# Performance work log

Hardware: AMD Instinct MI355X
Metric: run time of the kernel (lower is better)

## Reference

```python
import jax, jax.numpy as jnp
import numpy as np

K = 3
PAD = 1
DG = 4
GN_GROUPS = 32
EPS = 1e-5


def deform_conv2d(x, offset, weight):
    # x: [B,C,H,W], offset: [B,DG*2*K*K,H,W] (mmcv layout: per group, per kernel tap, (dy,dx))
    B, C, H, W = x.shape
    KK = K * K
    cg = C // DG
    dt = x.dtype
    off = offset.reshape(B, DG, KK, 2, H, W)
    dy, dx = off[:, :, :, 0], off[:, :, :, 1]  # [B,DG,KK,H,W]
    ky, kx = jnp.meshgrid(jnp.arange(K), jnp.arange(K), indexing='ij')
    ky = ky.reshape(KK).astype(dt)
    kx = kx.reshape(KK).astype(dt)
    hh = jnp.arange(H, dtype=dt)
    ww = jnp.arange(W, dtype=dt)
    # sampling coords: p0 + p_k + offset (stride 1, dilation 1)
    y = hh[None, None, None, :, None] - PAD + ky[None, None, :, None, None] + dy
    xs = ww[None, None, None, None, :] - PAD + kx[None, None, :, None, None] + dx
    y0 = jnp.floor(y)
    x0 = jnp.floor(xs)
    wy1 = y - y0
    wx1 = xs - x0
    xg = x.reshape(B, DG, cg, H * W)

    def corner(yi, xi):
        # zero padding outside the feature map
        valid = (yi >= 0) & (yi < H) & (xi >= 0) & (xi < W)
        yc = jnp.clip(yi, 0, H - 1).astype(jnp.int32)
        xc = jnp.clip(xi, 0, W - 1).astype(jnp.int32)
        idx = (yc * W + xc).reshape(B, DG, KK * H * W)
        v = jax.vmap(jax.vmap(lambda xf, ix: xf[:, ix]))(xg, idx)  # [B,DG,cg,KK*H*W]
        v = v.reshape(B, DG, cg, KK, H, W)
        return v * valid.astype(dt)[:, :, None]

    col = (corner(y0, x0) * ((1 - wy1) * (1 - wx1))[:, :, None]
           + corner(y0, x0 + 1) * ((1 - wy1) * wx1)[:, :, None]
           + corner(y0 + 1, x0) * (wy1 * (1 - wx1))[:, :, None]
           + corner(y0 + 1, x0 + 1) * (wy1 * wx1)[:, :, None])  # [B,DG,cg,KK,H,W]
    col = col.reshape(B, C, KK, H, W)
    O = weight.shape[0]
    return jnp.einsum('ock,bckhw->bohw', weight.reshape(O, C, KK), col)


def group_norm(x, gamma, beta):
    B, C, H, W = x.shape
    xg = x.reshape(B, GN_GROUPS, -1)
    m = xg.mean(-1, keepdims=True)
    v = xg.var(-1, keepdims=True)
    xn = ((xg - m) * jax.lax.rsqrt(v + EPS)).reshape(B, C, H, W)
    return xn * gamma[None, :, None, None] + beta[None, :, None, None]


def setup_inputs() -> dict:
    key = jax.random.key(0)
    k1, k2, k3, k4 = jax.random.split(key, 4)
    B, C, H, W = 4, 256, 64, 64
    x = jax.random.normal(k1, (B, C, H, W), dtype=jnp.float32)
    shape = jax.random.normal(k2, (B, 4, H, W), dtype=jnp.float32)
    w_offset = jax.random.normal(k3, (DG * 2 * K * K, 4), dtype=jnp.float32) * 0.01
    w_deform = jax.random.normal(k4, (C, C, K, K), dtype=jnp.float32) * 0.01
    gamma = jnp.ones((C,), jnp.float32)
    beta = jnp.zeros((C,), jnp.float32)
    return {"x": x, "shape": shape, "w_offset": w_offset, "w_deform": w_deform, "gamma": gamma, "beta": beta}


def reference(x, shape, w_offset, w_deform, gamma, beta):
    # conv_offset: 1x1 conv on detached `shape`
    offset = jnp.einsum('oi,bihw->bohw', w_offset, jax.lax.stop_gradient(shape))
    out = deform_conv2d(x, offset, w_deform)
    return jax.nn.relu(group_norm(out, gamma, beta))
```

## Files before the change

### kernel.cpp

```cpp
#include <hip/hip_runtime.h>
#include <stdint.h>

#define BB   4
#define CCH  256
#define HH   64
#define WWD  64
#define HWSZ 4096
#define DGRP 4
#define CG   64
#define KKN  9
#define KT   2304
#define NND  16384
#define GNG  32
#define EPSV 1e-5f

#define WS_COLT  0
#define WS_WB    75497472
#define WS_G     76677120
#define WS_PART  93454336

typedef __attribute__((ext_vector_type(8))) short short8;
typedef __attribute__((ext_vector_type(4))) float f32x4;

__device__ inline unsigned short f2bf(float f) {
    union { float f; unsigned u; } v; v.f = f;
    unsigned u = v.u;
    return (unsigned short)((u + 0x7FFFu + ((u >> 16) & 1u)) >> 16);
}

__device__ inline void gl_lds16(const void* g, void* l) {
    __builtin_amdgcn_global_load_lds(
        (const __attribute__((address_space(1))) void*)g,
        (__attribute__((address_space(3))) void*)l,
        16, 0, 0);
}

__global__ __launch_bounds__(256) void wconv_kernel(const float* __restrict__ wd,
                                                    unsigned short* __restrict__ Wb) {
    int idx = blockIdx.x * 256 + threadIdx.x;
    int o = idx / KT;
    int r = idx % KT;
    int kk = r >> 8;
    int c  = r & 255;
    Wb[idx] = f2bf(wd[o * KT + c * KKN + kk]);
}

__global__ __launch_bounds__(256) void col_kernel(const float* __restrict__ x,
                                                  const float* __restrict__ shp,
                                                  const float* __restrict__ woff,
                                                  unsigned short* __restrict__ colT) {
    __shared__ __align__(16) float xt[4 * 12 * 64 * 4];

    int bid   = blockIdx.x;
    int band  = bid & 7;
    int cq    = (bid >> 3) & 3;
    int dg    = (bid >> 5) & 3;
    int b     = bid >> 7;
    int h0    = band * 8;
    int tid   = threadIdx.x;
    int lane  = tid & 63;
    int wv    = tid >> 6;

    const float* xg = x + (size_t)(b * CCH + dg * CG + cq * 16) * HWSZ;
    #pragma unroll 1
    for (int ii = 0; ii < 6; ++ii) {
        float v[8]; int la[8];
        #pragma unroll
        for (int u = 0; u < 8; ++u) {
            int idx = (ii * 8 + u) * 256 + tid;
            int j   = idx / 768;
            int rem = idx - j * 768;
            int r   = rem >> 6;
            int w   = rem & 63;
            int gr  = min(max(h0 - 2 + r, 0), HH - 1);
            v[u]  = xg[(size_t)j * HWSZ + gr * 64 + w];
            la[u] = ((j >> 2) * 12 + r) * 256 + w * 4 + (j & 3);
        }
        #pragma unroll
        for (int u = 0; u < 8; ++u) xt[la[u]] = v[u];
    }
    __syncthreads();

    const char* xtb = (const char*)xt;

    #pragma unroll 1
    for (int hr = 0; hr < 2; ++hr) {
        int h  = h0 + wv * 2 + hr;
        int hw = h * 64 + lane;
        float s0 = shp[(b * 4 + 0) * HWSZ + hw];
        float s1 = shp[(b * 4 + 1) * HWSZ + hw];
        float s2 = shp[(b * 4 + 2) * HWSZ + hw];
        float s3 = shp[(b * 4 + 3) * HWSZ + hw];

        unsigned short* rowp = colT + (size_t)(b * HWSZ + hw) * KT + dg * CG + cq * 16;

        #pragma unroll
        for (int kk = 0; kk < KKN; ++kk) {
            const float* wo = woff + (dg * 18 + kk * 2) * 4;
            float dy = wo[0] * s0 + wo[1] * s1 + wo[2] * s2 + wo[3] * s3;
            float dx = wo[4] * s0 + wo[5] * s1 + wo[6] * s2 + wo[7] * s3;

            int ky = kk / 3, kx = kk % 3;
            float y  = (float)(h - 1 + ky) + dy;
            float xs = (float)(lane - 1 + kx) + dx;
            float y0f = floorf(y), x0f = floorf(xs);
            float wy1 = y - y0f,  wx1 = xs - x0f;
            float wy0 = 1.f - wy1, wx0 = 1.f - wx1;
            int iy0 = (int)y0f, ix0 = (int)x0f;
            int iy1 = iy0 + 1,  ix1 = ix0 + 1;
            bool vy0 = (iy0 >= 0) && (iy0 < HH);
            bool vy1 = (iy1 >= 0) && (iy1 < HH);
            bool vx0 = (ix0 >= 0) && (ix0 < WWD);
            bool vx1 = (ix1 >= 0) && (ix1 < WWD);
            float w00 = (vy0 && vx0) ? wy0 * wx0 : 0.f;
            float w01 = (vy0 && vx1) ? wy0 * wx1 : 0.f;
            float w10 = (vy1 && vx0) ? wy1 * wx0 : 0.f;
            float w11 = (vy1 && vx1) ? wy1 * wx1 : 0.f;
            int cy0 = min(max(iy0, 0), HH - 1);
            int cy1 = min(max(iy1, 0), HH - 1);
            int cx0 = min(max(ix0, 0), WWD - 1);
            int cx1 = min(max(ix1, 0), WWD - 1);
            int ty0 = min(max(cy0 - (h0 - 2), 0), 11);
            int ty1 = min(max(cy1 - (h0 - 2), 0), 11);
            int a00 = (ty0 * 64 + cx0) * 16;
            int a01 = (ty0 * 64 + cx1) * 16;
            int a10 = (ty1 * 64 + cx0) * 16;
            int a11 = (ty1 * 64 + cx1) * 16;

            unsigned short tmp[16];
            #pragma unroll
            for (int c4g = 0; c4g < 4; ++c4g) {
                int base = c4g * 12288;
                const float4 v00 = *(const float4*)(xtb + base + a00);
                const float4 v01 = *(const float4*)(xtb + base + a01);
                const float4 v10 = *(const float4*)(xtb + base + a10);
                const float4 v11 = *(const float4*)(xtb + base + a11);
                float rx = w00 * v00.x + w01 * v01.x + w10 * v10.x + w11 * v11.x;
                float ry = w00 * v00.y + w01 * v01.y + w10 * v10.y + w11 * v11.y;
                float rz = w00 * v00.z + w01 * v01.z + w10 * v10.z + w11 * v11.z;
                float rw = w00 * v00.w + w01 * v01.w + w10 * v10.w + w11 * v11.w;
                tmp[c4g * 4 + 0] = f2bf(rx);
                tmp[c4g * 4 + 1] = f2bf(ry);
                tmp[c4g * 4 + 2] = f2bf(rz);
                tmp[c4g * 4 + 3] = f2bf(rw);
            }
            uint4* dst = (uint4*)(rowp + kk * 256);
            const uint4* src = (const uint4*)tmp;
            dst[0] = src[0];
            dst[1] = src[1];
        }
    }
}

__global__ __launch_bounds__(256) void gemm_kernel(const unsigned short* __restrict__ Wb,
                                                   const unsigned short* __restrict__ colT,
                                                   float* __restrict__ G,
                                                   float* __restrict__ partials) {
    __shared__ __align__(16) short As[64 * 64];
    __shared__ __align__(16) short Bs[128 * 64];
    __shared__ float sred[16];

    int tid  = threadIdx.x;
    int lane = tid & 63;
    int wv   = tid >> 6;
    int wm   = wv >> 1;
    int wn   = wv & 1;

    int idx  = blockIdx.x;
    int xcd  = idx & 7;
    int j2   = idx >> 3;
    int n0   = (xcd * 16 + (j2 >> 2)) * 128;
    int m0   = (j2 & 3) * 64;

    if (tid < 16) sred[tid] = 0.f;

    int r_a = tid >> 3;
    int s_a = tid & 7;
    int k_a = (s_a ^ (r_a & 7)) * 8;

    f32x4 acc[2][4] = {};

    int quad = lane >> 4;
    int lrow = lane & 15;
    int sw   = lrow & 7;

    for (int kt = 0; kt < KT; kt += 64) {
        #pragma unroll
        for (int u = 0; u < 2; ++u) {
            int rr = u * 32 + r_a;
            gl_lds16(Wb + (size_t)(m0 + rr) * KT + kt + k_a,
                     (short*)As + (u * 256 + tid) * 8);
        }
        #pragma unroll
        for (int u = 0; u < 4; ++u) {
            int rr = u * 32 + r_a;
            gl_lds16(colT + (size_t)(n0 + rr) * KT + kt + k_a,
                     (short*)Bs + (u * 256 + tid) * 8);
        }
        __syncthreads();

        #pragma unroll
        for (int kb = 0; kb < 2; ++kb) {
            int slot = (kb * 4 + quad) ^ sw;
            short8 a[2], b[4];
            #pragma unroll
            for (int i = 0; i < 2; ++i)
                a[i] = *(const short8*)&As[(wm * 32 + i * 16 + lrow) * 64 + slot * 8];
            #pragma unroll
            for (int j = 0; j < 4; ++j)
                b[j] = *(const short8*)&Bs[(wn * 64 + j * 16 + lrow) * 64 + slot * 8];
            #pragma unroll
            for (int i = 0; i < 2; ++i)
                #pragma unroll
                for (int j = 0; j < 4; ++j)
                    acc[i][j] = __builtin_amdgcn_mfma_f32_16x16x32_bf16(a[i], b[j], acc[i][j], 0, 0, 0);
        }
        __syncthreads();
    }

    #pragma unroll
    for (int i = 0; i < 2; ++i) {
        int m = m0 + wm * 32 + i * 16 + quad * 4;
        #pragma unroll
        for (int j = 0; j < 4; ++j) {
            int n = n0 + wn * 64 + j * 16 + lrow;
            #pragma unroll
            for (int r = 0; r < 4; ++r)
                G[(size_t)(m + r) * NND + n] = acc[i][j][r];
        }
    }

    #pragma unroll
    for (int i = 0; i < 2; ++i) {
        float s1 = 0.f, s2 = 0.f;
        #pragma unroll
        for (int j = 0; j < 4; ++j)
            #pragma unroll
            for (int r = 0; r < 4; ++r) {
                float v = acc[i][j][r];
                s1 += v;
                s2 += v * v;
            }
        #pragma unroll
        for (int off = 1; off < 16; off <<= 1) {
            s1 += __shfl_xor(s1, off);
            s2 += __shfl_xor(s2, off);
        }
        if (lrow == 0) {
            int gg = (wm * 32 + i * 16 + quad * 4) >> 3;
            atomicAdd(&sred[gg * 2],     s1);
            atomicAdd(&sred[gg * 2 + 1], s2);
        }
    }
    __syncthreads();
    if (tid < 8) {
        int b  = n0 >> 12;
        int g0 = m0 >> 3;
        atomicAdd(&partials[(b * 32 + g0 + tid) * 2],     sred[tid * 2]);
        atomicAdd(&partials[(b * 32 + g0 + tid) * 2 + 1], sred[tid * 2 + 1]);
    }
}

__global__ __launch_bounds__(256) void gn_apply_kernel(const float* __restrict__ G,
                                                       const float* __restrict__ partials,
                                                       const float* __restrict__ gamma,
                                                       const float* __restrict__ beta,
                                                       float* __restrict__ out) {
    int idx = blockIdx.x * 256 + threadIdx.x;
    int hw4 = idx & 1023;
    int o   = (idx >> 10) & 255;
    int b   = idx >> 18;
    int g   = o >> 3;
    const float invN = 1.f / 32768.f;
    float p1 = partials[(b * 32 + g) * 2];
    float p2 = partials[(b * 32 + g) * 2 + 1];
    float mean = p1 * invN;
    float var  = p2 * invN - mean * mean;
    float rstd = rsqrtf(var + EPSV);
    float ga = gamma[o], be = beta[o];
    const float4 v = *(const float4*)&G[(size_t)o * NND + b * HWSZ + hw4 * 4];
    float4 r;
    r.x = fmaxf(0.f, (v.x - mean) * rstd * ga + be);
    r.y = fmaxf(0.f, (v.y - mean) * rstd * ga + be);
    r.z = fmaxf(0.f, (v.z - mean) * rstd * ga + be);
    r.w = fmaxf(0.f, (v.w - mean) * rstd * ga + be);
    *(float4*)&out[(size_t)(b * CCH + o) * HWSZ + hw4 * 4] = r;
}

extern "C" void kernel_launch(void* const* d_in, const int* in_sizes, int n_in,
                              void* d_out, int out_size, void* d_ws, size_t ws_size,
                              hipStream_t stream) {
    const float* x     = (const float*)d_in[0];
    const float* shp   = (const float*)d_in[1];
    const float* woff  = (const float*)d_in[2];
    const float* wdef  = (const float*)d_in[3];
    const float* gamma = (const float*)d_in[4];
    const float* beta  = (const float*)d_in[5];
    float* out = (float*)d_out;

    char* ws = (char*)d_ws;
    unsigned short* colT = (unsigned short*)(ws + WS_COLT);
    unsigned short* Wb   = (unsigned short*)(ws + WS_WB);
    float* G             = (float*)(ws + WS_G);
    float* partials      = (float*)(ws + WS_PART);

    hipMemsetAsync(partials, 0, 128 * 2 * sizeof(float), stream);
    wconv_kernel<<<2304, 256, 0, stream>>>(wdef, Wb);
    col_kernel<<<512, 256, 0, stream>>>(x, shp, woff, colT);
    gemm_kernel<<<512, 256, 0, stream>>>(Wb, colT, G, partials);
    gn_apply_kernel<<<4096, 256, 0, stream>>>(G, partials, gamma, beta, out);
}
```

Before: 147.1 us.

## Fuse weight conversion into col kernel, store x tile and GEMM output as bf16

```diff
diff --git a/kernel.cpp b/kernel.cpp
--- a/kernel.cpp
+++ b/kernel.cpp
@@ -28,6 +28,13 @@
     return (unsigned short)((u + 0x7FFFu + ((u >> 16) & 1u)) >> 16);
 }
 
+__device__ inline float bflo(unsigned u) {
+    union { unsigned u; float f; } v; v.u = u << 16; return v.f;
+}
+__device__ inline float bfhi(unsigned u) {
+    union { unsigned u; float f; } v; v.u = u & 0xffff0000u; return v.f;
+}
+
 __device__ inline void gl_lds16(const void* g, void* l) {
     __builtin_amdgcn_global_load_lds(
         (const __attribute__((address_space(1))) void*)g,
@@ -35,29 +42,38 @@
         16, 0, 0);
 }
 
-__global__ __launch_bounds__(256) void wconv_kernel(const float* __restrict__ wd,
-                                                    unsigned short* __restrict__ Wb) {
-    int idx = blockIdx.x * 256 + threadIdx.x;
-    int o = idx / KT;
-    int r = idx % KT;
-    int kk = r >> 8;
-    int c  = r & 255;
-    Wb[idx] = f2bf(wd[o * KT + c * KKN + kk]);
-}
-
 __global__ __launch_bounds__(256) void col_kernel(const float* __restrict__ x,
                                                   const float* __restrict__ shp,
                                                   const float* __restrict__ woff,
-                                                  unsigned short* __restrict__ colT) {
-    __shared__ __align__(16) float xt[4 * 12 * 64 * 4];
-
-    int bid   = blockIdx.x;
+                                                  unsigned short* __restrict__ colT,
+                                                  const float* __restrict__ wd,
+                                                  unsigned short* __restrict__ Wb) {
+    __shared__ __align__(16) unsigned short xt[4 * 12 * 64 * 4];
+
+    int bid = blockIdx.x;
+    int tid = threadIdx.x;
+
+    if (bid >= 512) {
+        int base = (bid - 512) * 1024 + tid * 4;
+        unsigned short t[4];
+        #pragma unroll
+        for (int u = 0; u < 4; ++u) {
+            int idx = base + u;
+            int o  = idx / KT;
+            int r  = idx % KT;
+            int kk = r >> 8;
+            int c  = r & 255;
+            t[u] = f2bf(wd[o * KT + c * KKN + kk]);
+        }
+        *(uint2*)&Wb[base] = *(const uint2*)t;
+        return;
+    }
+
     int band  = bid & 7;
     int cq    = (bid >> 3) & 3;
     int dg    = (bid >> 5) & 3;
     int b     = bid >> 7;
     int h0    = band * 8;
-    int tid   = threadIdx.x;
     int lane  = tid & 63;
     int wv    = tid >> 6;
 
@@ -77,7 +93,7 @@
             la[u] = ((j >> 2) * 12 + r) * 256 + w * 4 + (j & 3);
         }
         #pragma unroll
-        for (int u = 0; u < 8; ++u) xt[la[u]] = v[u];
+        for (int u = 0; u < 8; ++u) xt[la[u]] = f2bf(v[u]);
     }
     __syncthreads();
 
@@ -122,27 +138,27 @@
             int cx1 = min(max(ix1, 0), WWD - 1);
             int ty0 = min(max(cy0 - (h0 - 2), 0), 11);
             int ty1 = min(max(cy1 - (h0 - 2), 0), 11);
-            int a00 = (ty0 * 64 + cx0) * 16;
-            int a01 = (ty0 * 64 + cx1) * 16;
-            int a10 = (ty1 * 64 + cx0) * 16;
-            int a11 = (ty1 * 64 + cx1) * 16;
+            int a00 = (ty0 * 64 + cx0) * 8;
+            int a01 = (ty0 * 64 + cx1) * 8;
+            int a10 = (ty1 * 64 + cx0) * 8;
+            int a11 = (ty1 * 64 + cx1) * 8;
 
             unsigned short tmp[16];
             #pragma unroll
             for (int c4g = 0; c4g < 4; ++c4g) {
-                int base = c4g * 12288;
-                const float4 v00 = *(const float4*)(xtb + base + a00);
-                const float4 v01 = *(const float4*)(xtb + base + a01);
-                const float4 v10 = *(const float4*)(xtb + base + a10);
-                const float4 v11 = *(const float4*)(xtb + base + a11);
-                float rx = w00 * v00.x + w01 * v01.x + w10 * v10.x + w11 * v11.x;
-                float ry = w00 * v00.y + w01 * v01.y + w10 * v10.y + w11 * v11.y;
-                float rz = w00 * v00.z + w01 * v01.z + w10 * v10.z + w11 * v11.z;
-                float rw = w00 * v00.w + w01 * v01.w + w10 * v10.w + w11 * v11.w;
-                tmp[c4g * 4 + 0] = f2bf(rx);
-                tmp[c4g * 4 + 1] = f2bf(ry);
-                tmp[c4g * 4 + 2] = f2bf(rz);
-                tmp[c4g * 4 + 3] = f2bf(rw);
+                int base = c4g * 6144;
+                const uint2 q00 = *(const uint2*)(xtb + base + a00);
+                const uint2 q01 = *(const uint2*)(xtb + base + a01);
+                const uint2 q10 = *(const uint2*)(xtb + base + a10);
+                const uint2 q11 = *(const uint2*)(xtb + base + a11);
+                float r0 = w00 * bflo(q00.x) + w01 * bflo(q01.x) + w10 * bflo(q10.x) + w11 * bflo(q11.x);
+                float r1 = w00 * bfhi(q00.x) + w01 * bfhi(q01.x) + w10 * bfhi(q10.x) + w11 * bfhi(q11.x);
+                float r2 = w00 * bflo(q00.y) + w01 * bflo(q01.y) + w10 * bflo(q10.y) + w11 * bflo(q11.y);
+                float r3 = w00 * bfhi(q00.y) + w01 * bfhi(q01.y) + w10 * bfhi(q10.y) + w11 * bfhi(q11.y);
+                tmp[c4g * 4 + 0] = f2bf(r0);
+                tmp[c4g * 4 + 1] = f2bf(r1);
+                tmp[c4g * 4 + 2] = f2bf(r2);
+                tmp[c4g * 4 + 3] = f2bf(r3);
             }
             uint4* dst = (uint4*)(rowp + kk * 256);
             const uint4* src = (const uint4*)tmp;
@@ -154,7 +170,7 @@
 
 __global__ __launch_bounds__(256) void gemm_kernel(const unsigned short* __restrict__ Wb,
                                                    const unsigned short* __restrict__ colT,
-                                                   float* __restrict__ G,
+                                                   unsigned short* __restrict__ G,
                                                    float* __restrict__ partials) {
     __shared__ __align__(16) short As[64 * 64];
     __shared__ __align__(16) short Bs[128 * 64];
@@ -226,7 +242,7 @@
             int n = n0 + wn * 64 + j * 16 + lrow;
             #pragma unroll
             for (int r = 0; r < 4; ++r)
-                G[(size_t)(m + r) * NND + n] = acc[i][j][r];
+                G[(size_t)(m + r) * NND + n] = f2bf(acc[i][j][r]);
         }
     }
 
@@ -261,7 +277,7 @@
     }
 }
 
-__global__ __launch_bounds__(256) void gn_apply_kernel(const float* __restrict__ G,
+__global__ __launch_bounds__(256) void gn_apply_kernel(const unsigned short* __restrict__ G,
                                                        const float* __restrict__ partials,
                                                        const float* __restrict__ gamma,
                                                        const float* __restrict__ beta,
@@ -278,12 +294,12 @@
     float var  = p2 * invN - mean * mean;
     float rstd = rsqrtf(var + EPSV);
     float ga = gamma[o], be = beta[o];
-    const float4 v = *(const float4*)&G[(size_t)o * NND + b * HWSZ + hw4 * 4];
+    const uint2 q = *(const uint2*)&G[(size_t)o * NND + b * HWSZ + hw4 * 4];
     float4 r;
-    r.x = fmaxf(0.f, (v.x - mean) * rstd * ga + be);
-    r.y = fmaxf(0.f, (v.y - mean) * rstd * ga + be);
-    r.z = fmaxf(0.f, (v.z - mean) * rstd * ga + be);
-    r.w = fmaxf(0.f, (v.w - mean) * rstd * ga + be);
+    r.x = fmaxf(0.f, (bflo(q.x) - mean) * rstd * ga + be);
+    r.y = fmaxf(0.f, (bfhi(q.x) - mean) * rstd * ga + be);
+    r.z = fmaxf(0.f, (bflo(q.y) - mean) * rstd * ga + be);
+    r.w = fmaxf(0.f, (bfhi(q.y) - mean) * rstd * ga + be);
     *(float4*)&out[(size_t)(b * CCH + o) * HWSZ + hw4 * 4] = r;
 }
 
@@ -301,12 +317,11 @@
     char* ws = (char*)d_ws;
     unsigned short* colT = (unsigned short*)(ws + WS_COLT);
     unsigned short* Wb   = (unsigned short*)(ws + WS_WB);
-    float* G             = (float*)(ws + WS_G);
+    unsigned short* G    = (unsigned short*)(ws + WS_G);
     float* partials      = (float*)(ws + WS_PART);
 
     hipMemsetAsync(partials, 0, 128 * 2 * sizeof(float), stream);
-    wconv_kernel<<<2304, 256, 0, stream>>>(wdef, Wb);
-    col_kernel<<<512, 256, 0, stream>>>(x, shp, woff, colT);
+    col_kernel<<<1088, 256, 0, stream>>>(x, shp, woff, colT, wdef, Wb);
     gemm_kernel<<<512, 256, 0, stream>>>(Wb, colT, G, partials);
     gn_apply_kernel<<<4096, 256, 0, stream>>>(G, partials, gamma, beta, out);
 }
```

New measurement: 140.2 us. -4.7%, faster.
